# Kernel tuning notes

Hardware: AMD Instinct MI355X
Metric: run time of the kernel (lower is better)

The kernel has to match this reference:

```python
import jax, jax.numpy as jnp
import numpy as np

B, N, D = 256, 2048, 128
ANCHOR = 0


def setup_inputs() -> dict:
    key = jax.random.key(0)
    k0, k1, k2, k3 = jax.random.split(key, 4)
    return {
        "embs": jax.random.normal(k0, (B * N, D), jnp.float32),
        "W1": jax.random.normal(k1, (D, 2 * D), jnp.float32) / np.sqrt(2 * D),
        "b1": jnp.zeros((D,), jnp.float32),
        "W2": jax.random.normal(k2, (D, D), jnp.float32) / np.sqrt(D),
        "b2": jnp.zeros((D,), jnp.float32),
        "batch_idx": jax.random.randint(k3, (B * N,), 0, B, dtype=jnp.int32),
        "batch_size": B,
        "num_nodes": N,
        "num_anchors": ANCHOR,
    }


def reference(embs, W1, b1, W2, b2, batch_idx, batch_size, num_nodes, num_anchors):
    # static boolean mask over nodes (num_anchors is a Python int)
    non_target = np.arange(num_nodes) != num_anchors
    e = embs.reshape(batch_size, num_nodes, -1)            # (B, N, D)
    non_targets = e[:, non_target]                          # (B, N-1, D)
    target = e[:, ~non_target]                              # (B, 1, D)
    x = jnp.concatenate(
        (jnp.broadcast_to(target, non_targets.shape), non_targets), axis=-1
    )                                                       # (B, N-1, 2D)
    h = jax.nn.relu(jnp.einsum("bnk,dk->bnd", x, W1) + b1)  # (B, N-1, D)
    y = jnp.einsum("bnk,dk->bnd", h, W2) + b2               # (B, N-1, D)
    y = y.reshape(batch_size * (num_nodes - 1), -1)
    bidx = batch_idx.reshape(batch_size, num_nodes)[:, non_target].reshape(-1)
    return jax.ops.segment_sum(y, bidx, num_segments=batch_size)  # (B, D)
```

## Files before the change

### kernel.cpp

```cpp
#include <hip/hip_runtime.h>

#define B_SZ    256
#define N_NODES 2048
#define D_DIM   128
#define NROW_TOT (B_SZ * N_NODES)

typedef __attribute__((ext_vector_type(8))) short short8;
typedef __attribute__((ext_vector_type(4))) float f32x4;

#define WS_W1BF   0
#define WS_COUNT  65536
#define WS_OFF    66560
#define WS_CURSOR 67584
#define WS_ACC    83968
#define WS_P      215040
#define WS_NEEDED (WS_P + NROW_TOT * 4)

__device__ __forceinline__ unsigned pk2(float x, float y) {
    unsigned a = __float_as_uint(x), b = __float_as_uint(y);
    a += 0x7fffu + ((a >> 16) & 1u);
    b += 0x7fffu + ((b >> 16) & 1u);
    return (a >> 16) | (b & 0xffff0000u);
}

__global__ void k_prep_w1(const float* __restrict__ W1, unsigned* __restrict__ w1bf) {
    int i = blockIdx.x * 256 + threadIdx.x;
    float2 f = ((const float2*)W1)[i];
    w1bf[i] = pk2(f.x, f.y);
}

__global__ void k_hist(const int* __restrict__ bidx, int* __restrict__ count) {
    __shared__ int lh[256];
    int t = threadIdx.x;
    lh[t] = 0;
    __syncthreads();
    int base = blockIdx.x * 1024 + t * 4;
    int4 v = ((const int4*)bidx)[blockIdx.x * 256 + t];
    if (((base + 0) & 2047) != 0) atomicAdd(&lh[v.x], 1);
    if (((base + 1) & 2047) != 0) atomicAdd(&lh[v.y], 1);
    if (((base + 2) & 2047) != 0) atomicAdd(&lh[v.z], 1);
    if (((base + 3) & 2047) != 0) atomicAdd(&lh[v.w], 1);
    __syncthreads();
    if (lh[t]) atomicAdd(&count[t], lh[t]);
}

__global__ void k_scan(const int* __restrict__ count, int* __restrict__ off,
                       int* __restrict__ cursor) {
    __shared__ int sv[256];
    int t = threadIdx.x;
    sv[t] = count[t];
    __syncthreads();
    for (int o = 1; o < 256; o <<= 1) {
        int v = (t >= o) ? sv[t - o] : 0;
        __syncthreads();
        sv[t] += v;
        __syncthreads();
    }
    int ex = sv[t] - count[t];
    off[t] = ex;
    cursor[t * 16] = ex;
}

__global__ void k_scatter(const int* __restrict__ bidx, int* __restrict__ cursor,
                          int* __restrict__ P) {
    __shared__ int lh[256];
    __shared__ int sbase[256];
    int t = threadIdx.x;
    lh[t] = 0;
    __syncthreads();
    int base = blockIdx.x * 1024 + t * 4;
    int4 v = ((const int4*)bidx)[blockIdx.x * 256 + t];
    int p0 = -1, p1 = -1, p2 = -1, p3 = -1;
    if (((base + 0) & 2047) != 0) p0 = atomicAdd(&lh[v.x], 1);
    if (((base + 1) & 2047) != 0) p1 = atomicAdd(&lh[v.y], 1);
    if (((base + 2) & 2047) != 0) p2 = atomicAdd(&lh[v.z], 1);
    if (((base + 3) & 2047) != 0) p3 = atomicAdd(&lh[v.w], 1);
    __syncthreads();
    if (lh[t]) sbase[t] = atomicAdd(&cursor[t * 16], lh[t]);
    __syncthreads();
    if (p0 >= 0) P[sbase[v.x] + p0] = base + 0;
    if (p1 >= 0) P[sbase[v.y] + p1] = base + 1;
    if (p2 >= 0) P[sbase[v.z] + p2] = base + 2;
    if (p3 >= 0) P[sbase[v.w] + p3] = base + 3;
}

#define CHUNK   64
#define ESTRIDE 528

__global__ __launch_bounds__(1024) void k_main(
    const float* __restrict__ embs, const float* __restrict__ b1,
    const short* __restrict__ w1bf, const int* __restrict__ P,
    const int* __restrict__ off, const int* __restrict__ count,
    float* __restrict__ ACC)
{
    __shared__ char  estage[CHUNK * ESTRIDE];
    __shared__ float segacc[D_DIM];

    int tid = threadIdx.x;
    int s   = blockIdx.x;
    int cnt = count[s];
    int base = off[s];

    if (tid < D_DIM) segacc[tid] = 0.f;

    int lane = tid & 63;
    int wid  = tid >> 6;
    int rt   = wid & 3;
    int cg   = wid >> 2;
    int q    = lane >> 4;
    int i15  = lane & 15;

    short8 bfrag[8][2];
#pragma unroll
    for (int kt = 0; kt < 8; kt++)
#pragma unroll
        for (int ct = 0; ct < 2; ct++) {
            int n = cg * 32 + ct * 16 + i15;
            bfrag[kt][ct] = *(const short8*)(w1bf + n * 256 + kt * 32 + q * 8);
        }
    float b1c0 = b1[cg * 32 + i15];
    float b1c1 = b1[cg * 32 + 16 + i15];
    float asum0 = 0.f, asum1 = 0.f;

    int srow = tid >> 4;
    int part = tid & 15;
    __syncthreads();

    int nchunk = (cnt + CHUNK - 1) >> 6;
    for (int c = 0; c < nchunk; c++) {
        int rl = c * 64 + srow;
        int gr = base + (rl < cnt ? rl : cnt - 1);
        int ridx = P[gr];
        int b = ridx >> 11;
        const float4* src;
        if (part < 8) src = (const float4*)(embs + (b << 11) * D_DIM) + part * 4;
        else          src = (const float4*)(embs + ridx * D_DIM) + (part - 8) * 4;
        float4 f0 = src[0], f1 = src[1], f2 = src[2], f3 = src[3];
        unsigned u0 = pk2(f0.x, f0.y), u1 = pk2(f0.z, f0.w);
        unsigned u2 = pk2(f1.x, f1.y), u3 = pk2(f1.z, f1.w);
        unsigned u4 = pk2(f2.x, f2.y), u5 = pk2(f2.z, f2.w);
        unsigned u6 = pk2(f3.x, f3.y), u7 = pk2(f3.z, f3.w);
        uint4* dst = (uint4*)(estage + srow * ESTRIDE + part * 32);
        dst[0] = make_uint4(u0, u1, u2, u3);
        dst[1] = make_uint4(u4, u5, u6, u7);
        __syncthreads();

        f32x4 m0 = {0.f, 0.f, 0.f, 0.f}, m1 = {0.f, 0.f, 0.f, 0.f};
        const char* arow = estage + (rt * 16 + i15) * ESTRIDE + q * 16;
#pragma unroll
        for (int kt = 0; kt < 8; kt++) {
            short8 a = *(const short8*)(arow + kt * 64);
            m0 = __builtin_amdgcn_mfma_f32_16x16x32_bf16(a, bfrag[kt][0], m0, 0, 0, 0);
            m1 = __builtin_amdgcn_mfma_f32_16x16x32_bf16(a, bfrag[kt][1], m1, 0, 0, 0);
        }
        int rbase = c * 64 + rt * 16 + q * 4;
#pragma unroll
        for (int j = 0; j < 4; j++) {
            if (rbase + j < cnt) {
                asum0 += fmaxf(m0[j] + b1c0, 0.f);
                asum1 += fmaxf(m1[j] + b1c1, 0.f);
            }
        }
        __syncthreads();
    }

    asum0 += __shfl_xor(asum0, 16, 64);
    asum0 += __shfl_xor(asum0, 32, 64);
    asum1 += __shfl_xor(asum1, 16, 64);
    asum1 += __shfl_xor(asum1, 32, 64);
    if (lane < 16) {
        atomicAdd(&segacc[cg * 32 + lane],      asum0);
        atomicAdd(&segacc[cg * 32 + 16 + lane], asum1);
    }
    __syncthreads();
    if (tid < D_DIM) ACC[s * D_DIM + tid] = segacc[tid];
}

__global__ void k_out(const float* __restrict__ ACC, const float* __restrict__ W2,
                      const float* __restrict__ b2, const int* __restrict__ count,
                      float* __restrict__ out) {
    __shared__ float a[D_DIM];
    int s = blockIdx.x, d = threadIdx.x;
    a[d] = ACC[s * D_DIM + d];
    __syncthreads();
    float sum = (float)count[s] * b2[d];
    const float4* w = (const float4*)(W2 + d * D_DIM);
#pragma unroll
    for (int k = 0; k < 32; k++) {
        float4 wv = w[k];
        sum += a[4 * k + 0] * wv.x + a[4 * k + 1] * wv.y
             + a[4 * k + 2] * wv.z + a[4 * k + 3] * wv.w;
    }
    out[s * D_DIM + d] = sum;
}

extern "C" void kernel_launch(void* const* d_in, const int* in_sizes, int n_in,
                              void* d_out, int out_size, void* d_ws, size_t ws_size,
                              hipStream_t stream) {
    const float* embs = (const float*)d_in[0];
    const float* W1   = (const float*)d_in[1];
    const float* b1   = (const float*)d_in[2];
    const float* W2   = (const float*)d_in[3];
    const float* b2   = (const float*)d_in[4];
    const int*   bidx = (const int*)d_in[5];

    char* ws = (char*)d_ws;
    unsigned* w1bf_u = (unsigned*)(ws + WS_W1BF);
    short*    w1bf   = (short*)(ws + WS_W1BF);
    int*   count  = (int*)(ws + WS_COUNT);
    int*   off    = (int*)(ws + WS_OFF);
    int*   cursor = (int*)(ws + WS_CURSOR);
    float* ACC    = (float*)(ws + WS_ACC);
    int*   P      = (int*)(ws + WS_P);

    hipMemsetAsync(count, 0, 256 * sizeof(int), stream);
    k_prep_w1<<<64, 256, 0, stream>>>(W1, w1bf_u);
    k_hist<<<512, 256, 0, stream>>>(bidx, count);
    k_scan<<<1, 256, 0, stream>>>(count, off, cursor);
    k_scatter<<<512, 256, 0, stream>>>(bidx, cursor, P);
    k_main<<<256, 1024, 0, stream>>>(embs, b1, w1bf, P, off, count, ACC);
    k_out<<<256, 128, 0, stream>>>(ACC, W2, b2, count, (float*)d_out);
}
```

Measured before the change: 437.1 us.

## Fuse preprocessing into one kernel, cache targets in LDS, double-buffer node staging

Collapses the W1 conversion, histogram, scan and scatter kernels into one prep kernel. It does this by bucketing row indices into fixed-capacity per-segment slots (CAP=4096) rather than computing exact offsets. The main kernel now preloads all 256 target rows as bf16 into swizzled LDS, so staging only gathers the non-target half of each row. Staging is double-buffered, with the next chunk's global loads issued before the MFMA work and one barrier per chunk dropped. This cuts launch count and gather traffic, but relies on no segment exceeding CAP rows. It also uses about 100KB+ of LDS, which may limit occupancy.

```diff
diff --git a/kernel.cpp b/kernel.cpp
--- a/kernel.cpp
+++ b/kernel.cpp
@@ -10,11 +10,10 @@
 
 #define WS_W1BF   0
 #define WS_COUNT  65536
-#define WS_OFF    66560
-#define WS_CURSOR 67584
-#define WS_ACC    83968
-#define WS_P      215040
-#define WS_NEEDED (WS_P + NROW_TOT * 4)
+#define WS_ACC    66560
+#define WS_P      197632
+#define CAP       4096
+#define WS_NEEDED (WS_P + B_SZ * CAP * 4)
 
 __device__ __forceinline__ unsigned pk2(float x, float y) {
     unsigned a = __float_as_uint(x), b = __float_as_uint(y);
@@ -23,85 +22,67 @@
     return (a >> 16) | (b & 0xffff0000u);
 }
 
-__global__ void k_prep_w1(const float* __restrict__ W1, unsigned* __restrict__ w1bf) {
-    int i = blockIdx.x * 256 + threadIdx.x;
-    float2 f = ((const float2*)W1)[i];
-    w1bf[i] = pk2(f.x, f.y);
-}
-
-__global__ void k_hist(const int* __restrict__ bidx, int* __restrict__ count) {
+__global__ void k_prep(const float* __restrict__ W1, unsigned* __restrict__ w1bf,
+                       const int* __restrict__ bidx, int* __restrict__ count,
+                       int* __restrict__ P) {
+    if (blockIdx.x < 64) {
+        int i = blockIdx.x * 256 + threadIdx.x;
+        float2 f = ((const float2*)W1)[i];
+        w1bf[i] = pk2(f.x, f.y);
+        return;
+    }
     __shared__ int lh[256];
+    __shared__ int sbase[256];
+    int blk = blockIdx.x - 64;
     int t = threadIdx.x;
     lh[t] = 0;
     __syncthreads();
-    int base = blockIdx.x * 1024 + t * 4;
-    int4 v = ((const int4*)bidx)[blockIdx.x * 256 + t];
-    if (((base + 0) & 2047) != 0) atomicAdd(&lh[v.x], 1);
-    if (((base + 1) & 2047) != 0) atomicAdd(&lh[v.y], 1);
-    if (((base + 2) & 2047) != 0) atomicAdd(&lh[v.z], 1);
-    if (((base + 3) & 2047) != 0) atomicAdd(&lh[v.w], 1);
-    __syncthreads();
-    if (lh[t]) atomicAdd(&count[t], lh[t]);
-}
-
-__global__ void k_scan(const int* __restrict__ count, int* __restrict__ off,
-                       int* __restrict__ cursor) {
-    __shared__ int sv[256];
-    int t = threadIdx.x;
-    sv[t] = count[t];
-    __syncthreads();
-    for (int o = 1; o < 256; o <<= 1) {
-        int v = (t >= o) ? sv[t - o] : 0;
-        __syncthreads();
-        sv[t] += v;
-        __syncthreads();
-    }
-    int ex = sv[t] - count[t];
-    off[t] = ex;
-    cursor[t * 16] = ex;
-}
-
-__global__ void k_scatter(const int* __restrict__ bidx, int* __restrict__ cursor,
-                          int* __restrict__ P) {
-    __shared__ int lh[256];
-    __shared__ int sbase[256];
-    int t = threadIdx.x;
-    lh[t] = 0;
-    __syncthreads();
-    int base = blockIdx.x * 1024 + t * 4;
-    int4 v = ((const int4*)bidx)[blockIdx.x * 256 + t];
+    int base = blk * 1024 + t * 4;
+    int4 v = ((const int4*)bidx)[blk * 256 + t];
     int p0 = -1, p1 = -1, p2 = -1, p3 = -1;
     if (((base + 0) & 2047) != 0) p0 = atomicAdd(&lh[v.x], 1);
     if (((base + 1) & 2047) != 0) p1 = atomicAdd(&lh[v.y], 1);
     if (((base + 2) & 2047) != 0) p2 = atomicAdd(&lh[v.z], 1);
     if (((base + 3) & 2047) != 0) p3 = atomicAdd(&lh[v.w], 1);
     __syncthreads();
-    if (lh[t]) sbase[t] = atomicAdd(&cursor[t * 16], lh[t]);
-    __syncthreads();
-    if (p0 >= 0) P[sbase[v.x] + p0] = base + 0;
-    if (p1 >= 0) P[sbase[v.y] + p1] = base + 1;
-    if (p2 >= 0) P[sbase[v.z] + p2] = base + 2;
-    if (p3 >= 0) P[sbase[v.w] + p3] = base + 3;
+    if (lh[t]) sbase[t] = atomicAdd(&count[t], lh[t]);
+    __syncthreads();
+    if (p0 >= 0) P[v.x * CAP + sbase[v.x] + p0] = base + 0;
+    if (p1 >= 0) P[v.y * CAP + sbase[v.y] + p1] = base + 1;
+    if (p2 >= 0) P[v.z * CAP + sbase[v.z] + p2] = base + 2;
+    if (p3 >= 0) P[v.w * CAP + sbase[v.w] + p3] = base + 3;
 }
 
 #define CHUNK   64
-#define ESTRIDE 528
+#define ESTRIDE 272
 
 __global__ __launch_bounds__(1024) void k_main(
     const float* __restrict__ embs, const float* __restrict__ b1,
     const short* __restrict__ w1bf, const int* __restrict__ P,
-    const int* __restrict__ off, const int* __restrict__ count,
-    float* __restrict__ ACC)
+    const int* __restrict__ count, float* __restrict__ ACC)
 {
-    __shared__ char  estage[CHUNK * ESTRIDE];
+    __shared__ char  tgt[256 * 256];
+    __shared__ char  estage[2][CHUNK * ESTRIDE];
     __shared__ float segacc[D_DIM];
 
     int tid = threadIdx.x;
     int s   = blockIdx.x;
     int cnt = count[s];
-    int base = off[s];
+    const int pbase = s * CAP;
 
     if (tid < D_DIM) segacc[tid] = 0.f;
+
+#pragma unroll
+    for (int it = 0; it < 4; it++) {
+        int task = it * 1024 + tid;
+        int tr = task >> 4;
+        int p  = task & 15;
+        const float4* src = (const float4*)(embs + ((size_t)(tr << 11)) * D_DIM) + p * 2;
+        float4 g0 = src[0], g1 = src[1];
+        uint4 w = make_uint4(pk2(g0.x, g0.y), pk2(g0.z, g0.w),
+                             pk2(g1.x, g1.y), pk2(g1.z, g1.w));
+        *(uint4*)(tgt + ((tr * 256 + p * 16) ^ ((tr & 7) << 4))) = w;
+    }
 
     int lane = tid & 63;
     int wid  = tid >> 6;
@@ -122,36 +103,69 @@
     float b1c1 = b1[cg * 32 + 16 + i15];
     float asum0 = 0.f, asum1 = 0.f;
 
-    int srow = tid >> 4;
-    int part = tid & 15;
-    __syncthreads();
+    int srow = tid >> 3;
+    int part = tid & 7;
+    bool stager = tid < 512;
 
     int nchunk = (cnt + CHUNK - 1) >> 6;
+
+    float4 f0, f1, f2, f3;
+    int bcur = 0, ridx_next = 0;
+
+    if (nchunk > 0 && stager) {
+        int gr = pbase + (srow < cnt ? srow : cnt - 1);
+        int r0 = P[gr];
+        bcur = r0 >> 11;
+        const float4* src = (const float4*)(embs + (size_t)r0 * D_DIM) + part * 4;
+        f0 = src[0]; f1 = src[1]; f2 = src[2]; f3 = src[3];
+        if (nchunk > 1) {
+            int rl = CHUNK + srow;
+            ridx_next = P[pbase + (rl < cnt ? rl : cnt - 1)];
+        }
+    }
+    __syncthreads();
+
     for (int c = 0; c < nchunk; c++) {
-        int rl = c * 64 + srow;
-        int gr = base + (rl < cnt ? rl : cnt - 1);
-        int ridx = P[gr];
-        int b = ridx >> 11;
-        const float4* src;
-        if (part < 8) src = (const float4*)(embs + (b << 11) * D_DIM) + part * 4;
-        else          src = (const float4*)(embs + ridx * D_DIM) + (part - 8) * 4;
-        float4 f0 = src[0], f1 = src[1], f2 = src[2], f3 = src[3];
-        unsigned u0 = pk2(f0.x, f0.y), u1 = pk2(f0.z, f0.w);
-        unsigned u2 = pk2(f1.x, f1.y), u3 = pk2(f1.z, f1.w);
-        unsigned u4 = pk2(f2.x, f2.y), u5 = pk2(f2.z, f2.w);
-        unsigned u6 = pk2(f3.x, f3.y), u7 = pk2(f3.z, f3.w);
-        uint4* dst = (uint4*)(estage + srow * ESTRIDE + part * 32);
-        dst[0] = make_uint4(u0, u1, u2, u3);
-        dst[1] = make_uint4(u4, u5, u6, u7);
+        char* wb = estage[c & 1];
+        if (stager) {
+            uint4 wa = make_uint4(pk2(f0.x, f0.y), pk2(f0.z, f0.w),
+                                  pk2(f1.x, f1.y), pk2(f1.z, f1.w));
+            uint4 wbv = make_uint4(pk2(f2.x, f2.y), pk2(f2.z, f2.w),
+                                   pk2(f3.x, f3.y), pk2(f3.z, f3.w));
+            uint4* dst = (uint4*)(wb + srow * ESTRIDE + part * 32);
+            dst[0] = wa; dst[1] = wbv;
+            if (part == 0) *(int*)(wb + srow * ESTRIDE + 256) = bcur;
+        }
         __syncthreads();
 
+        if (stager && c + 1 < nchunk) {
+            int r = ridx_next;
+            bcur = r >> 11;
+            const float4* src = (const float4*)(embs + (size_t)r * D_DIM) + part * 4;
+            f0 = src[0]; f1 = src[1]; f2 = src[2]; f3 = src[3];
+            if (c + 2 < nchunk) {
+                int rl = (c + 2) * CHUNK + srow;
+                ridx_next = P[pbase + (rl < cnt ? rl : cnt - 1)];
+            }
+        }
+
         f32x4 m0 = {0.f, 0.f, 0.f, 0.f}, m1 = {0.f, 0.f, 0.f, 0.f};
-        const char* arow = estage + (rt * 16 + i15) * ESTRIDE + q * 16;
-#pragma unroll
-        for (int kt = 0; kt < 8; kt++) {
-            short8 a = *(const short8*)(arow + kt * 64);
+        int row = rt * 16 + i15;
+        int b = *(const int*)(wb + row * ESTRIDE + 256);
+        unsigned sw = ((unsigned)(b & 7)) << 4;
+        unsigned tb = ((unsigned)b << 8) + (unsigned)(q * 16);
+#pragma unroll
+        for (int kt = 0; kt < 4; kt++) {
+            short8 a = *(const short8*)(tgt + ((tb + kt * 64) ^ sw));
             m0 = __builtin_amdgcn_mfma_f32_16x16x32_bf16(a, bfrag[kt][0], m0, 0, 0, 0);
             m1 = __builtin_amdgcn_mfma_f32_16x16x32_bf16(a, bfrag[kt][1], m1, 0, 0, 0);
+        }
+        const char* ar = wb + row * ESTRIDE + q * 16;
+#pragma unroll
+        for (int kt = 0; kt < 4; kt++) {
+            short8 a = *(const short8*)(ar + kt * 64);
+            m0 = __builtin_amdgcn_mfma_f32_16x16x32_bf16(a, bfrag[kt + 4][0], m0, 0, 0, 0);
+            m1 = __builtin_amdgcn_mfma_f32_16x16x32_bf16(a, bfrag[kt + 4][1], m1, 0, 0, 0);
         }
         int rbase = c * 64 + rt * 16 + q * 4;
 #pragma unroll
@@ -161,7 +175,6 @@
                 asum1 += fmaxf(m1[j] + b1c1, 0.f);
             }
         }
-        __syncthreads();
     }
 
     asum0 += __shfl_xor(asum0, 16, 64);
@@ -208,16 +221,11 @@
     unsigned* w1bf_u = (unsigned*)(ws + WS_W1BF);
     short*    w1bf   = (short*)(ws + WS_W1BF);
     int*   count  = (int*)(ws + WS_COUNT);
-    int*   off    = (int*)(ws + WS_OFF);
-    int*   cursor = (int*)(ws + WS_CURSOR);
     float* ACC    = (float*)(ws + WS_ACC);
     int*   P      = (int*)(ws + WS_P);
 
     hipMemsetAsync(count, 0, 256 * sizeof(int), stream);
-    k_prep_w1<<<64, 256, 0, stream>>>(W1, w1bf_u);
-    k_hist<<<512, 256, 0, stream>>>(bidx, count);
-    k_scan<<<1, 256, 0, stream>>>(count, off, cursor);
-    k_scatter<<<512, 256, 0, stream>>>(bidx, cursor, P);
-    k_main<<<256, 1024, 0, stream>>>(embs, b1, w1bf, P, off, count, ACC);
+    k_prep<<<576, 256, 0, stream>>>(W1, w1bf_u, bidx, count, P);
+    k_main<<<256, 1024, 0, stream>>>(embs, b1, w1bf, P, count, ACC);
     k_out<<<256, 128, 0, stream>>>(ACC, W2, b2, count, (float*)d_out);
 }
```

Result: faster. 408.3 us (-6.6%).
